# Optimization experiments

Hardware: AMD Instinct MI355X
Metric: run time of the kernel (lower is better)

The kernel has to match this reference:

```python
import jax, jax.numpy as jnp
import numpy as np

NUM_GRAPHS = 512   # number of graphs in the batch
MAX_NODES = 192    # static pad bound (actual sizes are in [96,160])
TOTAL = 65536      # total atoms across all graphs
D = 256            # model dim (from MultiheadAttention(256, 4))
H = 4              # heads
DH = D // H        # head dim = 64


def setup_inputs() -> dict:
    # Ragged graph sizes that sum exactly to TOTAL (pairs 128+p / 128-p).
    rng = np.random.default_rng(0)
    p = rng.integers(0, 33, size=NUM_GRAPHS // 2)
    sizes = np.concatenate([128 + p, 128 - p])
    rng.shuffle(sizes)
    batch = np.repeat(np.arange(NUM_GRAPHS, dtype=np.int32), sizes)

    key = jax.random.key(0)
    ks = jax.random.split(key, 12)
    s = 0.02
    return {
        "x": jax.random.normal(ks[0], (TOTAL, D), jnp.float32),
        "batch": jnp.asarray(batch),
        # attn1 (torch MultiheadAttention packed in_proj + out_proj)
        "in_w1": jax.random.normal(ks[1], (3 * D, D), jnp.float32) * s,
        "in_b1": jnp.zeros((3 * D,), jnp.float32),
        "out_w1": jax.random.normal(ks[2], (D, D), jnp.float32) * s,
        "out_b1": jnp.zeros((D,), jnp.float32),
        # attn2
        "in_w2": jax.random.normal(ks[3], (3 * D, D), jnp.float32) * s,
        "in_b2": jnp.zeros((3 * D,), jnp.float32),
        "out_w2": jax.random.normal(ks[4], (D, D), jnp.float32) * s,
        "out_b2": jnp.zeros((D,), jnp.float32),
        # readout MLP: 256 -> 256 -> 128 -> 1 (dropout is identity in eval)
        "r_w1": jax.random.normal(ks[5], (256, 256), jnp.float32) * s,
        "r_b1": jnp.zeros((256,), jnp.float32),
        "r_w2": jax.random.normal(ks[6], (128, 256), jnp.float32) * s,
        "r_b2": jnp.zeros((128,), jnp.float32),
        "r_w3": jax.random.normal(ks[7], (1, 128), jnp.float32) * s,
        "r_b3": jnp.zeros((1,), jnp.float32),
    }


def _mha(xd, mask, in_w, in_b, out_w, out_b):
    # xd: [B, L, D], mask: [B, L] (True = valid key). torch MHA semantics.
    B, L, _ = xd.shape
    qkv = xd @ in_w.T + in_b                                  # [B, L, 3D]
    q, k, v = jnp.split(qkv, 3, axis=-1)
    split = lambda t: t.reshape(B, L, H, DH).transpose(0, 2, 1, 3)  # [B,H,L,DH]
    q, k, v = split(q), split(k), split(v)
    scores = jnp.einsum("bhqd,bhkd->bhqk", q, k) / jnp.sqrt(jnp.float32(DH))
    scores = jnp.where(mask[:, None, None, :], scores, -jnp.inf)
    attn = jax.nn.softmax(scores, axis=-1)                    # each graph has >=1 node
    o = jnp.einsum("bhqk,bhkd->bhqd", attn, v)                # [B,H,L,DH]
    o = o.transpose(0, 2, 1, 3).reshape(B, L, D)
    return o @ out_w.T + out_b


def reference(x, batch, in_w1, in_b1, out_w1, out_b1,
              in_w2, in_b2, out_w2, out_b2,
              r_w1, r_b1, r_w2, r_b2, r_w3, r_b3):
    # Scatter ragged atoms into a padded dense [B, MAX_NODES, D] block
    # (equivalent to the per-graph Python loop, but one fused pass).
    idx = jnp.arange(TOTAL)
    pos = idx - jnp.searchsorted(batch, batch, side="left")   # position within graph
    dense = jnp.zeros((NUM_GRAPHS, MAX_NODES, D), x.dtype).at[batch, pos].set(x)
    mask = jnp.zeros((NUM_GRAPHS, MAX_NODES), bool).at[batch, pos].set(True)

    h = _mha(dense, mask, in_w1, in_b1, out_w1, out_b1)
    h = _mha(h, mask, in_w2, in_b2, out_w2, out_b2)

    # masked mean-pool over valid nodes of each graph
    m = mask[..., None].astype(h.dtype)
    pooled = (h * m).sum(axis=1) / m.sum(axis=1)              # [B, D]

    h1 = jax.nn.relu(pooled @ r_w1.T + r_b1)                  # dropout = identity (eval)
    h2 = jax.nn.relu(h1 @ r_w2.T + r_b2)
    energy = h2 @ r_w3.T + r_b3                               # [B, 1]
    return energy[:, 0]                                       # (batch_size,)
```

## Files before the change

kernel.cpp:

```cpp
#include <hip/hip_runtime.h>
#include <math.h>

#define TOTAL 65536
#define NG 512
#define DMODEL 256
#define QKVLD 768

typedef __attribute__((ext_vector_type(8))) short bf16x8;
typedef __attribute__((ext_vector_type(4))) float f32x4;

__device__ inline ushort f2bf(float f) {
    unsigned int u = __float_as_uint(f);
    unsigned int r = (u + 0x7FFFu + ((u >> 16) & 1u)) >> 16;
    return (ushort)r;
}
__device__ inline float bf2f(ushort h) { return __uint_as_float(((unsigned int)h) << 16); }

__device__ __forceinline__ void llds16(const void* gptr, void* lptr) {
    __builtin_amdgcn_global_load_lds(
        (const __attribute__((address_space(1))) unsigned int*)gptr,
        (__attribute__((address_space(3))) unsigned int*)lptr, 16, 0, 0);
}

__global__ __launch_bounds__(256) void prep_kernel(
    const float* __restrict__ x, const float* __restrict__ in_w1,
    const float* __restrict__ in_w2, const float* __restrict__ out_w1,
    const float* __restrict__ out_b1, const float* __restrict__ in_b2,
    const int* __restrict__ batch,
    ushort* __restrict__ xb, ushort* __restrict__ Wb1,
    ushort* __restrict__ Wc2b, float* __restrict__ bc2, int* __restrict__ starts)
{
    const int b = blockIdx.x, t = threadIdx.x;
    if (b < 16384) {
        int i = b * 256 + t;
        float4 v = ((const float4*)x)[i];
        ushort4 u;
        u.x = f2bf(v.x); u.y = f2bf(v.y); u.z = f2bf(v.z); u.w = f2bf(v.w);
        ((ushort4*)xb)[i] = u;
    } else if (b < 16576) {
        int i = (b - 16384) * 256 + t;
        float4 v = ((const float4*)in_w1)[i];
        ushort4 u;
        u.x = f2bf(v.x); u.y = f2bf(v.y); u.z = f2bf(v.z); u.w = f2bf(v.w);
        ((ushort4*)Wb1)[i] = u;
    } else if (b < 17344) {
        const int n = b - 16576;
        __shared__ float wrow[256];
        wrow[t] = in_w2[n * 256 + t];
        __syncthreads();
        float s = 0.f;
#pragma unroll 8
        for (int j = 0; j < 256; ++j) s += wrow[j] * out_w1[j * 256 + t];
        Wc2b[n * 256 + t] = f2bf(s);
    } else if (b < 17347) {
        int n = (b - 17344) * 256 + t;
        if (n < 768) {
            float s = 0.f;
            for (int j = 0; j < 256; ++j) s += in_w2[n * 256 + j] * out_b1[j];
            bc2[n] = s + in_b2[n];
        }
    } else {
        int g = (b - 17347) * 256 + t;
        if (g < NG) {
            int lo = 0, hi = TOTAL;
            while (lo < hi) {
                int mid = (lo + hi) >> 1;
                if (batch[mid] < g) lo = mid + 1; else hi = mid;
            }
            starts[g] = lo;
            if (g == 0) starts[NG] = TOTAL;
        }
    }
}

__global__ __launch_bounds__(256) void gemm_mfma(
    const ushort* __restrict__ A,
    const ushort* __restrict__ W,
    const float* __restrict__ bias,
    ushort* __restrict__ C, int ldc)
{
    __shared__ ushort As[128 * 64];
    __shared__ ushort Bs[128 * 64];
    const int tid = threadIdx.x;
    const int lane = tid & 63, wid = tid >> 6;
    const int grp = lane >> 4, ln16 = lane & 15;
    const int wm = wid & 1, wn = wid >> 1;

    const int bid = blockIdx.x;
    const int xcd = bid & 7;
    const int j6  = bid >> 3;
    const int mt  = xcd * 64 + j6 / 6;
    const int nt  = j6 % 6;
    const int n0 = nt * 128, m0 = mt * 128;

    const int lrow = lane >> 3;
    const int lchunk = (lane & 7) ^ lrow;

    f32x4 acc[4][4];
#pragma unroll
    for (int i = 0; i < 4; ++i)
#pragma unroll
        for (int j = 0; j < 4; ++j) acc[i][j] = (f32x4){0.f, 0.f, 0.f, 0.f};

    for (int k0 = 0; k0 < 256; k0 += 64) {
#pragma unroll
        for (int j = 0; j < 4; ++j) {
            int band = wid * 32 + j * 8;
            int row = band + lrow;
            llds16(A + (size_t)(m0 + row) * 256 + k0 + lchunk * 8, &As[band * 64]);
            llds16(W + (size_t)(n0 + row) * 256 + k0 + lchunk * 8, &Bs[band * 64]);
        }
        __syncthreads();
#pragma unroll
        for (int kc = 0; kc < 2; ++kc) {
            bf16x8 a[4], b[4];
#pragma unroll
            for (int i = 0; i < 4; ++i) {
                int r = wm * 64 + i * 16 + ln16;
                int p = (kc * 4 + grp) ^ (r & 7);
                a[i] = *(const bf16x8*)&As[r * 64 + p * 8];
            }
#pragma unroll
            for (int j = 0; j < 4; ++j) {
                int r = wn * 64 + j * 16 + ln16;
                int p = (kc * 4 + grp) ^ (r & 7);
                b[j] = *(const bf16x8*)&Bs[r * 64 + p * 8];
            }
#pragma unroll
            for (int i = 0; i < 4; ++i)
#pragma unroll
                for (int j = 0; j < 4; ++j)
                    acc[i][j] = __builtin_amdgcn_mfma_f32_16x16x32_bf16(a[i], b[j], acc[i][j], 0, 0, 0);
        }
        __syncthreads();
    }

#pragma unroll
    for (int j = 0; j < 4; ++j) {
        int col = n0 + wn * 64 + j * 16 + ln16;
        float bv = bias[col];
#pragma unroll
        for (int i = 0; i < 4; ++i) {
            int r0 = m0 + wm * 64 + i * 16 + grp * 4;
#pragma unroll
            for (int reg = 0; reg < 4; ++reg)
                C[(size_t)(r0 + reg) * ldc + col] = f2bf(acc[i][j][reg] + bv);
        }
    }
}

#define VLD 168
#define PLD 40

__global__ __launch_bounds__(512) void attn_mfma(const ushort* __restrict__ qkv,
                                                 ushort* __restrict__ obuf,
                                                 float* __restrict__ psumOut,
                                                 const int* __restrict__ starts) {
    __shared__ ushort Ks[160 * 64];
    __shared__ ushort Vt[64 * VLD];
    __shared__ ushort Ps[8 * 16 * PLD];
    __shared__ float  red[8][64];
    const int bid = blockIdx.x;
    const int xcd = bid & 7;
    const int j6  = bid >> 3;
    const int g = xcd * 64 + (j6 & 63);
    const int h = j6 >> 6;
    int s = starts[g];
    int e = starts[g + 1];
    s = (s < 0) ? 0 : ((s > TOTAL) ? TOTAL : s);
    e = (e < s) ? s : ((e > TOTAL) ? TOTAL : e);
    int L = e - s;
    if (L > 160) L = 160;
    if (L < 1) L = 1;
    const int ktL = (L + 15) >> 4;
    const int tid = threadIdx.x;
    const int lane = tid & 63, wid = tid >> 6;
    const int grp = lane >> 4, ln16 = lane & 15;
    const int lrow = lane >> 3;
    const int lchunk = (lane & 7) ^ lrow;

#pragma unroll
    for (int r = 0; r < 3; ++r) {
        int bi = r * 8 + wid;
        if (bi < 20) {
            int band = bi * 8;
            int row = band + lrow;
            int crow = (row < L) ? row : (L - 1);
            llds16(qkv + (size_t)(s + crow) * QKVLD + 256 + h * 64 + lchunk * 8, &Ks[band * 64]);
        }
    }
#pragma unroll
    for (int r = 0; r < 3; ++r) {
        int idx = r * 512 + tid;
        if (idx < 1280) {
            int kc = idx >> 6;
            int d = idx & 63;
            ushort tmp[8];
#pragma unroll
            for (int j = 0; j < 8; ++j) {
                int key = kc * 8 + j;
                int ckey = (key < L) ? key : (L - 1);
                tmp[j] = qkv[(size_t)(s + ckey) * QKVLD + 512 + h * 64 + d];
            }
            *(uint4*)&Vt[d * VLD + kc * 8] = *(const uint4*)tmp;
        }
    }
    __syncthreads();

    ushort* myP = &Ps[wid * 16 * PLD];
    float psum[4] = {0.f, 0.f, 0.f, 0.f};
    const bool pooled = (psumOut != nullptr);

    for (int q0 = wid * 16; q0 < L; q0 += 128) {
        bf16x8 qa[2];
        {
            int qi = q0 + ln16;
            int grow = (qi < L) ? (s + qi) : s;
            const ushort* qbase = qkv + (size_t)grow * QKVLD + h * 64;
            qa[0] = *(const bf16x8*)(qbase + grp * 8);
            qa[1] = *(const bf16x8*)(qbase + 32 + grp * 8);
        }
        f32x4 sc[10];
#pragma unroll
        for (int kt = 0; kt < 10; ++kt) {
            if (kt < ktL) {
                int row = kt * 16 + ln16;
                int p0 = grp ^ (row & 7);
                int p1 = (4 + grp) ^ (row & 7);
                bf16x8 b0 = *(const bf16x8*)&Ks[row * 64 + p0 * 8];
                bf16x8 b1 = *(const bf16x8*)&Ks[row * 64 + p1 * 8];
                f32x4 z = (f32x4){0.f, 0.f, 0.f, 0.f};
                z = __builtin_amdgcn_mfma_f32_16x16x32_bf16(qa[0], b0, z, 0, 0, 0);
                z = __builtin_amdgcn_mfma_f32_16x16x32_bf16(qa[1], b1, z, 0, 0, 0);
                sc[kt] = z;
            }
        }
        float sm[4] = {0.f, 0.f, 0.f, 0.f};
#pragma unroll
        for (int kt = 0; kt < 10; ++kt) {
            if (kt < ktL) {
                bool dead = (kt * 16 + ln16) >= L;
#pragma unroll
                for (int r = 0; r < 4; ++r) {
                    float p = __expf(dead ? -INFINITY : sc[kt][r] * 0.125f);
                    sc[kt][r] = p;
                    sm[r] += p;
                }
            } else {
#pragma unroll
                for (int r = 0; r < 4; ++r) sc[kt][r] = 0.f;
            }
        }
#pragma unroll
        for (int m = 1; m <= 8; m <<= 1)
#pragma unroll
            for (int r = 0; r < 4; ++r) sm[r] += __shfl_xor(sm[r], m, 64);
        float inv[4];
#pragma unroll
        for (int r = 0; r < 4; ++r) inv[r] = 1.f / sm[r];

        f32x4 o[4];
#pragma unroll
        for (int dt = 0; dt < 4; ++dt) o[dt] = (f32x4){0.f, 0.f, 0.f, 0.f};
#pragma unroll
        for (int st = 0; st < 5; ++st) {
            if (st * 32 < L) {
#pragma unroll
                for (int kti = 0; kti < 2; ++kti) {
                    int kt = st * 2 + kti;
#pragma unroll
                    for (int r = 0; r < 4; ++r)
                        myP[(grp * 4 + r) * PLD + kti * 16 + ln16] = f2bf(sc[kt][r]);
                }
                bf16x8 pa = *(const bf16x8*)&myP[ln16 * PLD + grp * 8];
#pragma unroll
                for (int dt = 0; dt < 4; ++dt) {
                    bf16x8 vb = *(const bf16x8*)&Vt[(dt * 16 + ln16) * VLD + st * 32 + grp * 8];
                    o[dt] = __builtin_amdgcn_mfma_f32_16x16x32_bf16(pa, vb, o[dt], 0, 0, 0);
                }
            }
        }
        if (pooled) {
#pragma unroll
            for (int dt = 0; dt < 4; ++dt)
#pragma unroll
                for (int reg = 0; reg < 4; ++reg) {
                    int q = q0 + grp * 4 + reg;
                    if (q < L) psum[dt] += o[dt][reg] * inv[reg];
                }
        } else {
#pragma unroll
            for (int dt = 0; dt < 4; ++dt)
#pragma unroll
                for (int reg = 0; reg < 4; ++reg) {
                    int q = q0 + grp * 4 + reg;
                    if (q < L)
                        obuf[(size_t)(s + q) * DMODEL + h * 64 + dt * 16 + ln16] =
                            f2bf(o[dt][reg] * inv[reg]);
                }
        }
    }

    if (pooled) {
#pragma unroll
        for (int dt = 0; dt < 4; ++dt) {
            psum[dt] += __shfl_xor(psum[dt], 16, 64);
            psum[dt] += __shfl_xor(psum[dt], 32, 64);
        }
        if (grp == 0) {
#pragma unroll
            for (int dt = 0; dt < 4; ++dt) red[wid][dt * 16 + ln16] = psum[dt];
        }
        __syncthreads();
        if (tid < 64) {
            float v = 0.f;
#pragma unroll
            for (int w = 0; w < 8; ++w) v += red[w][tid];
            psumOut[g * DMODEL + h * 64 + tid] = v;
        }
    }
}

__global__ __launch_bounds__(256) void readout_kernel(
    const float* __restrict__ psum, const int* __restrict__ starts,
    const float* __restrict__ ow2, const float* __restrict__ ob2,
    const float* __restrict__ w1, const float* __restrict__ b1,
    const float* __restrict__ w2, const float* __restrict__ b2,
    const float* __restrict__ w3, const float* __restrict__ b3,
    float* __restrict__ out)
{
    __shared__ float xs[256], ps[256], h1s[256], h2s[128];
    const int g = blockIdx.x, t = threadIdx.x;
    int s = starts[g], e = starts[g + 1];
    s = (s < 0) ? 0 : ((s > TOTAL) ? TOTAL : s);
    e = (e < s) ? s : ((e > TOTAL) ? TOTAL : e);
    int L = e - s;
    if (L < 1) L = 1;
    xs[t] = psum[g * 256 + t] / (float)L;
    __syncthreads();
    {
        const float* wr = ow2 + t * 256;
        float s0 = 0.f;
#pragma unroll 8
        for (int i = 0; i < 256; ++i) s0 += xs[i] * wr[i];
        ps[t] = s0 + ob2[t];
    }
    __syncthreads();
    {
        const float* wr = w1 + t * 256;
        float s0 = 0.f;
#pragma unroll 8
        for (int i = 0; i < 256; ++i) s0 += ps[i] * wr[i];
        float v = s0 + b1[t];
        h1s[t] = v > 0.f ? v : 0.f;
    }
    __syncthreads();
    if (t < 128) {
        const float* wr = w2 + t * 256;
        float s0 = 0.f;
#pragma unroll 8
        for (int i = 0; i < 256; ++i) s0 += h1s[i] * wr[i];
        float v = s0 + b2[t];
        h2s[t] = v > 0.f ? v : 0.f;
    }
    __syncthreads();
    if (t < 64) {
        float v = h2s[t] * w3[t] + h2s[t + 64] * w3[t + 64];
#pragma unroll
        for (int off = 32; off > 0; off >>= 1) v += __shfl_down(v, off, 64);
        if (t == 0) out[g] = v + b3[0];
    }
}

__global__ __launch_bounds__(256) void zero_out_kernel(float* __restrict__ out, int n) {
    int i = blockIdx.x * 256 + threadIdx.x;
    if (i < n) out[i] = 0.f;
}

extern "C" void kernel_launch(void* const* d_in, const int* in_sizes, int n_in,
                              void* d_out, int out_size, void* d_ws, size_t ws_size,
                              hipStream_t stream) {
    float* out = (float*)d_out;

    const int expect[16] = {
        TOTAL * DMODEL, TOTAL,
        3 * DMODEL * DMODEL, 3 * DMODEL,
        DMODEL * DMODEL, DMODEL,
        3 * DMODEL * DMODEL, 3 * DMODEL,
        DMODEL * DMODEL, DMODEL,
        256 * 256, 256,
        128 * 256, 128,
        128, 1
    };
    const size_t NEEDED = 135536640ull;
    bool ok = (n_in == 16) && (out_size == NG) && (d_ws != nullptr) && (ws_size >= NEEDED);
    if (ok) {
        for (int i = 0; i < 16; ++i)
            if (in_sizes[i] != expect[i]) { ok = false; break; }
    }
    if (!ok) {
        zero_out_kernel<<<(out_size + 255) / 256, 256, 0, stream>>>(out, out_size);
        return;
    }

    const float* x      = (const float*)d_in[0];
    const int*   batch  = (const int*)d_in[1];
    const float* in_w1  = (const float*)d_in[2];
    const float* in_b1  = (const float*)d_in[3];
    const float* out_w1 = (const float*)d_in[4];
    const float* out_b1 = (const float*)d_in[5];
    const float* in_w2  = (const float*)d_in[6];
    const float* in_b2  = (const float*)d_in[7];
    const float* out_w2 = (const float*)d_in[8];
    const float* out_b2 = (const float*)d_in[9];
    const float* r_w1   = (const float*)d_in[10];
    const float* r_b1   = (const float*)d_in[11];
    const float* r_w2   = (const float*)d_in[12];
    const float* r_b2   = (const float*)d_in[13];
    const float* r_w3   = (const float*)d_in[14];
    const float* r_b3   = (const float*)d_in[15];

    char* ws = (char*)d_ws;
    int*    starts = (int*)(ws + 0);
    float*  bc2    = (float*)(ws + 4096);
    float*  psum   = (float*)(ws + 8192);
    ushort* Wc2b   = (ushort*)(ws + 532480);
    ushort* Wb1    = (ushort*)(ws + 925696);
    ushort* bufO   = (ushort*)(ws + 1318912);
    ushort* bufQKV = (ushort*)(ws + 34873344ull);

    prep_kernel<<<17349, 256, 0, stream>>>(x, in_w1, in_w2, out_w1, out_b1, in_b2,
                                           batch, bufO, Wb1, Wc2b, bc2, starts);

    gemm_mfma<<<3072, 256, 0, stream>>>(bufO, Wb1, in_b1, bufQKV, QKVLD);
    attn_mfma<<<2048, 512, 0, stream>>>(bufQKV, bufO, nullptr, starts);

    gemm_mfma<<<3072, 256, 0, stream>>>(bufO, Wc2b, bc2, bufQKV, QKVLD);
    attn_mfma<<<2048, 512, 0, stream>>>(bufQKV, bufO, psum, starts);

    readout_kernel<<<NG, 256, 0, stream>>>(psum, starts, out_w2, out_b2,
                                           r_w1, r_b1, r_w2, r_b2, r_w3, r_b3, out);
}
```

Baseline: 332.6 us.

## Batch four graphs per readout block and coalesce weight reads with float4

The readout kernel now processes four graphs per block, so each weight row is loaded once and reused across four inputs. Weight rows are read as float4 by 16 lanes cooperating on one output, followed by a shuffle reduction, instead of each thread walking its own row in a strided, uncoalesced way. This cuts weight traffic and improves coalescing in the small readout MLP. The cost is fewer blocks (128) and extra shuffle work.

```diff
diff --git a/kernel.cpp b/kernel.cpp
--- a/kernel.cpp
+++ b/kernel.cpp
@@ -329,46 +329,124 @@
     const float* __restrict__ w3, const float* __restrict__ b3,
     float* __restrict__ out)
 {
-    __shared__ float xs[256], ps[256], h1s[256], h2s[128];
-    const int g = blockIdx.x, t = threadIdx.x;
-    int s = starts[g], e = starts[g + 1];
-    s = (s < 0) ? 0 : ((s > TOTAL) ? TOTAL : s);
-    e = (e < s) ? s : ((e > TOTAL) ? TOTAL : e);
-    int L = e - s;
-    if (L < 1) L = 1;
-    xs[t] = psum[g * 256 + t] / (float)L;
+    __shared__ float xs[4][256], ps[4][256], h1s[4][256], h2s[4][128];
+    const int t = threadIdx.x;
+    const int lane = t & 63, wid = t >> 6;
+    const int l16 = lane & 15, gq = lane >> 4;
+    const int g0 = blockIdx.x * 4;
+
+#pragma unroll
+    for (int g = 0; g < 4; ++g) {
+        int gg = g0 + g;
+        int s = starts[gg], e = starts[gg + 1];
+        s = (s < 0) ? 0 : ((s > TOTAL) ? TOTAL : s);
+        e = (e < s) ? s : ((e > TOTAL) ? TOTAL : e);
+        int L = e - s;
+        if (L < 1) L = 1;
+        xs[g][t] = psum[gg * 256 + t] / (float)L;
+    }
     __syncthreads();
+
+#pragma unroll 2
+    for (int o = 0; o < 16; ++o) {
+        int tt = wid * 64 + o * 4 + gq;
+        const float4* wrow = (const float4*)(ow2 + tt * 256);
+        float a0 = 0.f, a1 = 0.f, a2 = 0.f, a3 = 0.f;
+#pragma unroll
+        for (int k = 0; k < 4; ++k) {
+            float4 wv = wrow[l16 + k * 16];
+            float4 x0 = ((const float4*)xs[0])[l16 + k * 16];
+            float4 x1 = ((const float4*)xs[1])[l16 + k * 16];
+            float4 x2 = ((const float4*)xs[2])[l16 + k * 16];
+            float4 x3 = ((const float4*)xs[3])[l16 + k * 16];
+            a0 += wv.x * x0.x + wv.y * x0.y + wv.z * x0.z + wv.w * x0.w;
+            a1 += wv.x * x1.x + wv.y * x1.y + wv.z * x1.z + wv.w * x1.w;
+            a2 += wv.x * x2.x + wv.y * x2.y + wv.z * x2.z + wv.w * x2.w;
+            a3 += wv.x * x3.x + wv.y * x3.y + wv.z * x3.z + wv.w * x3.w;
+        }
+#pragma unroll
+        for (int m = 1; m <= 8; m <<= 1) {
+            a0 += __shfl_xor(a0, m, 64);
+            a1 += __shfl_xor(a1, m, 64);
+            a2 += __shfl_xor(a2, m, 64);
+            a3 += __shfl_xor(a3, m, 64);
+        }
+        if (l16 < 4) {
+            float v = (l16 & 1) ? ((l16 & 2) ? a3 : a1) : ((l16 & 2) ? a2 : a0);
+            ps[l16][tt] = v + ob2[tt];
+        }
+    }
+    __syncthreads();
+
+#pragma unroll 2
+    for (int o = 0; o < 16; ++o) {
+        int tt = wid * 64 + o * 4 + gq;
+        const float4* wrow = (const float4*)(w1 + tt * 256);
+        float a0 = 0.f, a1 = 0.f, a2 = 0.f, a3 = 0.f;
+#pragma unroll
+        for (int k = 0; k < 4; ++k) {
+            float4 wv = wrow[l16 + k * 16];
+            float4 x0 = ((const float4*)ps[0])[l16 + k * 16];
+            float4 x1 = ((const float4*)ps[1])[l16 + k * 16];
+            float4 x2 = ((const float4*)ps[2])[l16 + k * 16];
+            float4 x3 = ((const float4*)ps[3])[l16 + k * 16];
+            a0 += wv.x * x0.x + wv.y * x0.y + wv.z * x0.z + wv.w * x0.w;
+            a1 += wv.x * x1.x + wv.y * x1.y + wv.z * x1.z + wv.w * x1.w;
+            a2 += wv.x * x2.x + wv.y * x2.y + wv.z * x2.z + wv.w * x2.w;
+            a3 += wv.x * x3.x + wv.y * x3.y + wv.z * x3.z + wv.w * x3.w;
+        }
+#pragma unroll
+        for (int m = 1; m <= 8; m <<= 1) {
+            a0 += __shfl_xor(a0, m, 64);
+            a1 += __shfl_xor(a1, m, 64);
+            a2 += __shfl_xor(a2, m, 64);
+            a3 += __shfl_xor(a3, m, 64);
+        }
+        if (l16 < 4) {
+            float v = (l16 & 1) ? ((l16 & 2) ? a3 : a1) : ((l16 & 2) ? a2 : a0);
+            v += b1[tt];
+            h1s[l16][tt] = v > 0.f ? v : 0.f;
+        }
+    }
+    __syncthreads();
+
+#pragma unroll 2
+    for (int o = 0; o < 8; ++o) {
+        int tt = wid * 32 + o * 4 + gq;
+        const float4* wrow = (const float4*)(w2 + tt * 256);
+        float a0 = 0.f, a1 = 0.f, a2 = 0.f, a3 = 0.f;
+#pragma unroll
+        for (int k = 0; k < 4; ++k) {
+            float4 wv = wrow[l16 + k * 16];
+            float4 x0 = ((const float4*)h1s[0])[l16 + k * 16];
+            float4 x1 = ((const float4*)h1s[1])[l16 + k * 16];
+            float4 x2 = ((const float4*)h1s[2])[l16 + k * 16];
+            float4 x3 = ((const float4*)h1s[3])[l16 + k * 16];
+            a0 += wv.x * x0.x + wv.y * x0.y + wv.z * x0.z + wv.w * x0.w;
+            a1 += wv.x * x1.x + wv.y * x1.y + wv.z * x1.z + wv.w * x1.w;
+            a2 += wv.x * x2.x + wv.y * x2.y + wv.z * x2.z + wv.w * x2.w;
+            a3 += wv.x * x3.x + wv.y * x3.y + wv.z * x3.z + wv.w * x3.w;
+        }
+#pragma unroll
+        for (int m = 1; m <= 8; m <<= 1) {
+            a0 += __shfl_xor(a0, m, 64);
+            a1 += __shfl_xor(a1, m, 64);
+            a2 += __shfl_xor(a2, m, 64);
+            a3 += __shfl_xor(a3, m, 64);
+        }
+        if (l16 < 4) {
+            float v = (l16 & 1) ? ((l16 & 2) ? a3 : a1) : ((l16 & 2) ? a2 : a0);
+            v += b2[tt];
+            h2s[l16][tt] = v > 0.f ? v : 0.f;
+        }
+    }
+    __syncthreads();
+
     {
-        const float* wr = ow2 + t * 256;
-        float s0 = 0.f;
-#pragma unroll 8
-        for (int i = 0; i < 256; ++i) s0 += xs[i] * wr[i];
-        ps[t] = s0 + ob2[t];
-    }
-    __syncthreads();
-    {
-        const float* wr = w1 + t * 256;
-        float s0 = 0.f;
-#pragma unroll 8
-        for (int i = 0; i < 256; ++i) s0 += ps[i] * wr[i];
-        float v = s0 + b1[t];
-        h1s[t] = v > 0.f ? v : 0.f;
-    }
-    __syncthreads();
-    if (t < 128) {
-        const float* wr = w2 + t * 256;
-        float s0 = 0.f;
-#pragma unroll 8
-        for (int i = 0; i < 256; ++i) s0 += h1s[i] * wr[i];
-        float v = s0 + b2[t];
-        h2s[t] = v > 0.f ? v : 0.f;
-    }
-    __syncthreads();
-    if (t < 64) {
-        float v = h2s[t] * w3[t] + h2s[t + 64] * w3[t + 64];
-#pragma unroll
-        for (int off = 32; off > 0; off >>= 1) v += __shfl_down(v, off, 64);
-        if (t == 0) out[g] = v + b3[0];
+        float v = h2s[wid][lane] * w3[lane] + h2s[wid][lane + 64] * w3[lane + 64];
+#pragma unroll
+        for (int m = 1; m <= 32; m <<= 1) v += __shfl_xor(v, m, 64);
+        if (lane == 0) out[g0 + wid] = v + b3[0];
     }
 }
 
@@ -438,6 +516,6 @@
     gemm_mfma<<<3072, 256, 0, stream>>>(bufO, Wc2b, bc2, bufQKV, QKVLD);
     attn_mfma<<<2048, 512, 0, stream>>>(bufQKV, bufO, psum, starts);
 
-    readout_kernel<<<NG, 256, 0, stream>>>(psum, starts, out_w2, out_b2,
-                                           r_w1, r_b1, r_w2, r_b2, r_w3, r_b3, out);
-}
+    readout_kernel<<<NG / 4, 256, 0, stream>>>(psum, starts, out_w2, out_b2,
+                                               r_w1, r_b1, r_w2, r_b2, r_w3, r_b3, out);
+}
```

Result: no change. 327.4 us (-1.6%).
